# Kernel optimization log

Measured on AMD Instinct MI355X. Metric: run time of the kernel, lower is better.

Reference implementation:

```python
import jax, jax.numpy as jnp
import numpy as np

DIM = 640
HEADS = 8
HEAD_DIM = 80
CROSS = 768
FF_INNER = 4 * DIM  # 2560
EPS = 1e-5
SCALE = HEAD_DIM ** -0.5


def _ln(x, w, b):
    m = jnp.mean(x, axis=-1, keepdims=True)
    v = jnp.var(x, axis=-1, keepdims=True)
    return (x - m) * jax.lax.rsqrt(v + EPS) * w + b


def _split_heads(x):  # [B,S,D] -> [B,H,S,dh]
    B, S, D = x.shape
    return x.reshape(B, S, HEADS, D // HEADS).transpose(0, 2, 1, 3)


def _merge_heads(x):  # [B,H,S,dh] -> [B,S,D]
    B, H, S, dh = x.shape
    return x.transpose(0, 2, 1, 3).reshape(B, S, H * dh)


def _mha(q, k, v):
    # q:[B,S,D] k,v:[B,Skv,D]
    qh, kh, vh = _split_heads(q), _split_heads(k), _split_heads(v)
    scores = jnp.einsum('bhqd,bhkd->bhqk', qh, kh) * SCALE
    probs = jax.nn.softmax(scores, axis=-1)
    out = jnp.einsum('bhqk,bhkd->bhqd', probs, vh)
    return _merge_heads(out)


def _forward(hidden_states, encoder_hidden_states, video_length, p):
    BF, S, D = hidden_states.shape
    f = video_length
    b = BF // f

    # ---- attn1: sparse causal self-attention ----
    x = _ln(hidden_states, p['ln1_w'], p['ln1_b'])
    q = x @ p['q1']
    k = x @ p['k1']
    v = x @ p['v1']
    former = jnp.concatenate([jnp.zeros((1,), jnp.int32), jnp.arange(f - 1, dtype=jnp.int32)])
    def gather_kv(t):  # [BF,S,D] -> [BF,2S,D]
        t = t.reshape(b, f, S, D)
        first = jnp.broadcast_to(t[:, 0:1], (b, f, S, D))
        prev = t[:, former]
        return jnp.concatenate([first, prev], axis=2).reshape(BF, 2 * S, D)
    k = gather_kv(k)
    v = gather_kv(v)
    attn1 = _mha(q, k, v) @ p['o1_w'] + p['o1_b']
    hidden_states = attn1 + hidden_states

    # ---- attn2: cross attention to text ----
    x = _ln(hidden_states, p['ln2_w'], p['ln2_b'])
    q = x @ p['q2']
    k = encoder_hidden_states @ p['k2']
    v = encoder_hidden_states @ p['v2']
    attn2 = _mha(q, k, v) @ p['o2_w'] + p['o2_b']
    hidden_states = attn2 + hidden_states

    # ---- feed-forward (geglu) ----
    x = _ln(hidden_states, p['ln3_w'], p['ln3_b'])
    proj = x @ p['ff_w1'] + p['ff_b1']
    h, gate = jnp.split(proj, 2, axis=-1)
    ff = (h * jax.nn.gelu(gate)) @ p['ff_w2'] + p['ff_b2']
    return ff + hidden_states


def setup_inputs() -> dict:
    key = jax.random.key(0)
    ks = jax.random.split(key, 20)
    s = lambda i, shape, scale=0.02: jax.random.normal(ks[i], shape, jnp.float32) * scale
    inp = {
        'hidden_states': jax.random.normal(ks[0], (8, 1024, DIM), jnp.float32),
        'encoder_hidden_states': jax.random.normal(ks[1], (8, 77, CROSS), jnp.float32),
        'video_length': 8,
        'ln1_w': jnp.ones((DIM,)), 'ln1_b': jnp.zeros((DIM,)),
        'q1': s(2, (DIM, DIM)), 'k1': s(3, (DIM, DIM)), 'v1': s(4, (DIM, DIM)),
        'o1_w': s(5, (DIM, DIM)), 'o1_b': jnp.zeros((DIM,)),
        'ln2_w': jnp.ones((DIM,)), 'ln2_b': jnp.zeros((DIM,)),
        'q2': s(6, (DIM, DIM)), 'k2': s(7, (CROSS, DIM)), 'v2': s(8, (CROSS, DIM)),
        'o2_w': s(9, (DIM, DIM)), 'o2_b': jnp.zeros((DIM,)),
        'ln3_w': jnp.ones((DIM,)), 'ln3_b': jnp.zeros((DIM,)),
        'ff_w1': s(10, (DIM, 2 * FF_INNER)), 'ff_b1': jnp.zeros((2 * FF_INNER,)),
        'ff_w2': s(11, (FF_INNER, DIM)), 'ff_b2': jnp.zeros((DIM,)),
    }
    return inp


def reference(hidden_states, encoder_hidden_states, video_length,
              ln1_w, ln1_b, q1, k1, v1, o1_w, o1_b,
              ln2_w, ln2_b, q2, k2, v2, o2_w, o2_b,
              ln3_w, ln3_b, ff_w1, ff_b1, ff_w2, ff_b2):
    p = dict(ln1_w=ln1_w, ln1_b=ln1_b, q1=q1, k1=k1, v1=v1, o1_w=o1_w, o1_b=o1_b,
             ln2_w=ln2_w, ln2_b=ln2_b, q2=q2, k2=k2, v2=v2, o2_w=o2_w, o2_b=o2_b,
             ln3_w=ln3_w, ln3_b=ln3_b, ff_w1=ff_w1, ff_b1=ff_b1, ff_w2=ff_w2, ff_b2=ff_b2)
    return _forward(hidden_states, encoder_hidden_states, video_length, p)
```

## Files before the change

kernel.cpp:

```cpp
#include <hip/hip_runtime.h>
#include <stdint.h>

#define TOK   8192
#define DIM   640
#define HEADS 8
#define HD    80
#define SEQ   1024
#define CROSS 768
#define ETOK  616
#define FFI   2560
#define SCALE 0.11180339887498949f

typedef unsigned short u16;
typedef unsigned int   u32;

using bf8   = __attribute__((ext_vector_type(8))) short;
using f32x4 = __attribute__((ext_vector_type(4))) float;

struct __align__(16) U4 { u32 x, y, z, w; };
struct __align__(8)  U2 { u32 x, y; };

__device__ __forceinline__ float bf2f(u16 u){
  union { u32 i; float f; } v; v.i = ((u32)u) << 16; return v.f;
}
__device__ __forceinline__ u16 f2bf(float f){
  union { float f; u32 i; } v; v.f = f;
  u32 r = v.i + 0x7fffu + ((v.i >> 16) & 1u);
  return (u16)(r >> 16);
}
__device__ __forceinline__ u32 cvtpk_bf16(float lo, float hi){
  u32 r; asm("v_cvt_pk_bf16_f32 %0, %1, %2" : "=v"(r) : "v"(lo), "v"(hi)); return r;
}
__device__ __forceinline__ float gelu_t(float x){
  float y = 0.7978845608028654f * (x + 0.044715f * x * x * x);
  float e = __expf(2.f * y);
  return 0.5f * x * (2.f - 2.f / (e + 1.f));
}

__device__ __forceinline__ void gl2lds16(const u16* g, u16* l){
  __builtin_amdgcn_global_load_lds(
      (const __attribute__((address_space(1))) void*)g,
      (__attribute__((address_space(3))) void*)l, 16, 0, 0);
}

__global__ void zero_k(u16* p){ p[threadIdx.x] = 0; }

struct CvtJob  { const float* s; u16* d; int n; };
struct CvtJobs { CvtJob j[11]; };
__global__ __launch_bounds__(256) void cvt_all(CvtJobs jobs)
{
  const CvtJob jb = jobs.j[blockIdx.y];
  for (long i = (long)blockIdx.x*256 + threadIdx.x; i < jb.n; i += (long)gridDim.x*256)
    jb.d[i] = f2bf(jb.s[i]);
}

struct TJob  { const float* s; u16* d; int R, C, srcLd, dstLd; };
struct TJobs { TJob j[10]; };
__global__ __launch_bounds__(256) void transpose_tiled(TJobs jobs)
{
  const TJob jb = jobs.j[blockIdx.y];
  const int tilesC = jb.C >> 6;
  const int nt = (jb.R >> 6) * tilesC;
  if ((int)blockIdx.x >= nt) return;
  const int tr = (blockIdx.x / tilesC) << 6, tc = (blockIdx.x % tilesC) << 6;
  __shared__ u16 t[64][65];
  const int tid = threadIdx.x;
  const int rr = tid >> 3, c8 = (tid & 7) * 8;
  #pragma unroll
  for (int p = 0; p < 2; ++p){
    const int r = rr + p*32;
    const float* s = &jb.s[(long)(tr + r)*jb.srcLd + tc + c8];
    #pragma unroll
    for (int j = 0; j < 8; ++j) t[r][c8 + j] = f2bf(s[j]);
  }
  __syncthreads();
  #pragma unroll
  for (int p = 0; p < 2; ++p){
    const int c = rr + p*32;
    u16 tmp[8];
    #pragma unroll
    for (int j = 0; j < 8; ++j) tmp[j] = t[c8 + j][c];
    *(U4*)&jb.d[(long)(tc + c)*jb.dstLd + tr + c8] = *(U4*)tmp;
  }
}

__global__ __launch_bounds__(256) void transpose_tile(
    const u16* __restrict__ src, u16* __restrict__ dst,
    int srcLd, int dstLd)
{
  __shared__ u16 t[64][65];
  const int tr = blockIdx.y << 6, tc = blockIdx.x << 6;
  const int tid = threadIdx.x;
  const int rr = tid >> 3, c8 = (tid & 7) * 8;
  #pragma unroll
  for (int p = 0; p < 2; ++p){
    const int r = rr + p*32;
    U4 v = *(const U4*)&src[(long)(tr + r)*srcLd + tc + c8];
    const u16* pv = (const u16*)&v;
    #pragma unroll
    for (int j = 0; j < 8; ++j) t[r][c8 + j] = pv[j];
  }
  __syncthreads();
  #pragma unroll
  for (int p = 0; p < 2; ++p){
    const int c = rr + p*32;
    u16 tmp[8];
    #pragma unroll
    for (int j = 0; j < 8; ++j) tmp[j] = t[c8 + j][c];
    *(U4*)&dst[(long)(tc + c)*dstLd + tr + c8] = *(U4*)tmp;
  }
}

__global__ __launch_bounds__(256) void transpose_v2(
    const u16* __restrict__ src, u16* __restrict__ dst)
{
  int idx = blockIdx.x*256 + threadIdx.x;
  if (idx >= DIM*640) return;
  int d = idx / 640, c = idx - d*640;
  int g = c / 80, j = c - g*80;
  u16 v = 0;
  if (j < 77) v = src[(long)(g*77 + j)*(2*DIM) + DIM + d];
  dst[(long)d*640 + c] = v;
}

__global__ __launch_bounds__(256) void ln_k(
    const void* __restrict__ src, const u16* __restrict__ w,
    const u16* __restrict__ b, u16* __restrict__ dst, int srcf32)
{
  __shared__ float xr[DIM];
  __shared__ float red[256];
  const int tid = threadIdx.x;
  const long row = blockIdx.x;
  float ls = 0.f;
  for (int i = tid; i < DIM; i += 256){
    float v = srcf32 ? ((const float*)src)[row*DIM + i]
                     : bf2f(((const u16*)src)[row*DIM + i]);
    xr[i] = v; ls += v;
  }
  red[tid] = ls; __syncthreads();
  for (int o = 128; o > 0; o >>= 1){ if (tid < o) red[tid] += red[tid+o]; __syncthreads(); }
  const float mean = red[0] * (1.f/DIM);
  __syncthreads();
  float lq = 0.f;
  for (int i = tid; i < DIM; i += 256){ float d = xr[i] - mean; lq += d*d; }
  red[tid] = lq; __syncthreads();
  for (int o = 128; o > 0; o >>= 1){ if (tid < o) red[tid] += red[tid+o]; __syncthreads(); }
  const float var = red[0] * (1.f/DIM);
  const float rs = rsqrtf(var + 1e-5f);
  u16* q = dst + row*DIM;
  for (int i = tid; i < DIM; i += 256)
    q[i] = f2bf((xr[i] - mean)*rs*bf2f(w[i]) + bf2f(b[i]));
}

template<int BN>
__global__ __launch_bounds__(256) void gemm_bt(
    const u16* __restrict__ A, const u16* __restrict__ BT, void* __restrict__ C,
    int M, int N, int K, int lda, int ldb, int ldc,
    const u16* __restrict__ bias, const void* __restrict__ res, int ldr,
    int resf32, int outf32)
{
  constexpr int NT  = BN/32;
  constexpr int BCH = BN/16;
  constexpr int BPW = BCH/4;
  __shared__ __align__(16) u16 sA[2][8*512];
  __shared__ __align__(16) u16 sB[2][BCH*512];
  const int tid  = threadIdx.x;
  const int wave = tid >> 6, lane = tid & 63;
  const int quad = lane >> 4, l16 = lane & 15;
  const int m0 = blockIdx.y * 128, n0 = blockIdx.x * BN;
  const int wm = (wave >> 1) * 64, wn = (wave & 1) * (BN/2);
  const int srow = lane & 15;
  const int scol = (lane >> 4) * 8;

  long aoff[2];
  #pragma unroll
  for (int i = 0; i < 2; ++i){
    int r = m0 + (wave*2 + i)*16 + srow;
    r = r < M ? r : M - 1;
    aoff[i] = (long)r*lda + scol;
  }
  long boff[BPW];
  #pragma unroll
  for (int i = 0; i < BPW; ++i){
    int r = n0 + (wave*BPW + i)*16 + srow;
    boff[i] = (long)r*ldb + scol;
  }

  f32x4 acc[4][NT] = {};
  #pragma unroll
  for (int i = 0; i < 2; ++i)   gl2lds16(&A[aoff[i]],  &sA[0][(wave*2 + i)*512]);
  #pragma unroll
  for (int i = 0; i < BPW; ++i) gl2lds16(&BT[boff[i]], &sB[0][(wave*BPW + i)*512]);
  __syncthreads();

  int cur = 0;
  for (int k0 = 0; ; ){
    const int kn = k0 + 32;
    if (kn < K){
      #pragma unroll
      for (int i = 0; i < 2; ++i)   gl2lds16(&A[aoff[i] + kn],  &sA[cur^1][(wave*2 + i)*512]);
      #pragma unroll
      for (int i = 0; i < BPW; ++i) gl2lds16(&BT[boff[i] + kn], &sB[cur^1][(wave*BPW + i)*512]);
    }
    bf8 a[4], b[NT];
    #pragma unroll
    for (int mt = 0; mt < 4; ++mt)  a[mt] = *(const bf8*)&sA[cur][((wm>>4) + mt)*512 + lane*8];
    #pragma unroll
    for (int nt = 0; nt < NT; ++nt) b[nt] = *(const bf8*)&sB[cur][((wn>>4) + nt)*512 + lane*8];
    #pragma unroll
    for (int mt = 0; mt < 4; ++mt)
      #pragma unroll
      for (int nt = 0; nt < NT; ++nt)
        acc[mt][nt] = __builtin_amdgcn_mfma_f32_16x16x32_bf16(a[mt], b[nt], acc[mt][nt], 0, 0, 0);
    k0 = kn;
    if (k0 >= K) break;
    __syncthreads();
    cur ^= 1;
  }
  #pragma unroll
  for (int mt = 0; mt < 4; ++mt){
    const int rl = wm + mt*16 + quad*4;
    #pragma unroll
    for (int nt = 0; nt < NT; ++nt){
      const int col = n0 + wn + nt*16 + l16;
      float bv = bias ? bf2f(bias[col]) : 0.f;
      #pragma unroll
      for (int r = 0; r < 4; ++r){
        int row = m0 + rl + r;
        if (row < M){
          float v = acc[mt][nt][r] + bv;
          if (res) v += resf32 ? ((const float*)res)[(long)row*ldr + col]
                               : bf2f(((const u16*)res)[(long)row*ldr + col]);
          if (outf32) ((float*)C)[(long)row*ldc + col] = v;
          else        ((u16*)C) [(long)row*ldc + col] = f2bf(v);
        }
      }
    }
  }
}

__global__ __launch_bounds__(256) void gemm_geglu(
    const u16* __restrict__ A, const u16* __restrict__ W, u16* __restrict__ C,
    const u16* __restrict__ bias)
{
  __shared__ __align__(16) u16 sA[2][8*512];
  __shared__ __align__(16) u16 sH[2][4*512];
  __shared__ __align__(16) u16 sG[2][4*512];
  const int tid  = threadIdx.x;
  const int wave = tid >> 6, lane = tid & 63;
  const int quad = lane >> 4, l16 = lane & 15;
  const int m0 = blockIdx.y * 128, n0 = blockIdx.x * 64;
  const int wm = (wave >> 1) * 64, wn = (wave & 1) * 32;
  const int srow = lane & 15;
  const int scol = (lane >> 4) * 8;

  long aoff[2];
  #pragma unroll
  for (int i = 0; i < 2; ++i)
    aoff[i] = (long)(m0 + (wave*2 + i)*16 + srow)*DIM + scol;
  const long hoff = (long)(n0 + wave*16 + srow)*DIM + scol;
  const long goff = (long)(FFI + n0 + wave*16 + srow)*DIM + scol;

  f32x4 ah[4][2] = {}, ag[4][2] = {};
  #pragma unroll
  for (int i = 0; i < 2; ++i) gl2lds16(&A[aoff[i]], &sA[0][(wave*2 + i)*512]);
  gl2lds16(&W[hoff], &sH[0][wave*512]);
  gl2lds16(&W[goff], &sG[0][wave*512]);
  __syncthreads();

  int cur = 0;
  for (int k0 = 0; ; ){
    const int kn = k0 + 32;
    if (kn < DIM){
      #pragma unroll
      for (int i = 0; i < 2; ++i) gl2lds16(&A[aoff[i] + kn], &sA[cur^1][(wave*2 + i)*512]);
      gl2lds16(&W[hoff + kn], &sH[cur^1][wave*512]);
      gl2lds16(&W[goff + kn], &sG[cur^1][wave*512]);
    }
    bf8 a[4];
    #pragma unroll
    for (int mt = 0; mt < 4; ++mt) a[mt] = *(const bf8*)&sA[cur][((wm>>4) + mt)*512 + lane*8];
    #pragma unroll
    for (int nt = 0; nt < 2; ++nt){
      bf8 bh = *(const bf8*)&sH[cur][((wn>>4) + nt)*512 + lane*8];
      bf8 bg = *(const bf8*)&sG[cur][((wn>>4) + nt)*512 + lane*8];
      #pragma unroll
      for (int mt = 0; mt < 4; ++mt){
        ah[mt][nt] = __builtin_amdgcn_mfma_f32_16x16x32_bf16(a[mt], bh, ah[mt][nt], 0, 0, 0);
        ag[mt][nt] = __builtin_amdgcn_mfma_f32_16x16x32_bf16(a[mt], bg, ag[mt][nt], 0, 0, 0);
      }
    }
    k0 = kn;
    if (k0 >= DIM) break;
    __syncthreads();
    cur ^= 1;
  }
  #pragma unroll
  for (int mt = 0; mt < 4; ++mt){
    const int rl = wm + mt*16 + quad*4;
    #pragma unroll
    for (int nt = 0; nt < 2; ++nt){
      const int col = n0 + wn + nt*16 + l16;
      const float bh = bf2f(bias[col]);
      const float bg = bf2f(bias[FFI + col]);
      #pragma unroll
      for (int r = 0; r < 4; ++r){
        int row = m0 + rl + r;
        float h = ah[mt][nt][r] + bh;
        float g = ag[mt][nt][r] + bg;
        C[(long)row*FFI + col] = f2bf(h * gelu_t(g));
      }
    }
  }
}

template<int MODE>
__global__ __launch_bounds__(256) void attn_k(
    const u16* __restrict__ qbuf, const u16* __restrict__ kbuf,
    const u16* __restrict__ vT, u16* __restrict__ out,
    const u16* __restrict__ zblk)
{
  constexpr int QLD  = MODE ? DIM      : 3*DIM;
  constexpr int KLD  = MODE ? 2*DIM    : 3*DIM;
  constexpr int KCOL = MODE ? 0        : DIM;
  constexpr int VLD  = MODE ? DIM      : TOK;
  constexpr int NK   = MODE ? 77       : 2*SEQ;
  constexpr int NCH  = MODE ? 3        : 64;
  constexpr float C1   = SCALE * 1.4426950408889634f;
  constexpr float THRR = 8.0f / C1;

  const int qt = blockIdx.x, h = blockIdx.y, g = blockIdx.z;
  const int tid = threadIdx.x, wave = tid >> 6, lane = tid & 63;
  const int quad = lane >> 4, l16 = lane & 15;

  __shared__ __align__(16) u16 Qs[64*104];
  __shared__ __align__(16) u16 Kb[6*512];
  __shared__ __align__(16) u16 Vb[5*512];
  __shared__ __align__(16) u16 Ps[4][16*40];

  const int qrow0 = g*SEQ + qt*64;
  for (int v = tid; v < 640; v += 256){
    int r = v/10, c8 = (v - r*10)*8;
    *(U4*)&Qs[r*104 + c8] = *(const U4*)&qbuf[(long)(qrow0 + r)*QLD + h*HD + c8];
  }
  for (int v = tid; v < 128; v += 256){
    U4 z = {0,0,0,0};
    *(U4*)&Qs[(v>>1)*104 + 80 + (v&1)*8] = z;
  }
  __syncthreads();

  bf8 qf[3];
  #pragma unroll
  for (int ks = 0; ks < 3; ++ks)
    qf[ks] = *(const bf8*)&Qs[(wave*16 + l16)*104 + ks*32 + quad*8];

  const int former = (g == 0) ? 0 : (g - 1);

  auto stage = [&](int c){
    int krow0, vrow0;
    if (MODE == 0){
      int kb = c*32;
      int fr = (kb >> 10) ? former : 0;
      krow0 = fr*SEQ + (kb & (SEQ-1));
      vrow0 = krow0;
    } else {
      krow0 = c*32;
      vrow0 = g*80 + c*32;
    }
    #pragma unroll
    for (int ci = 0; ci < 6; ++ci){
      if ((ci & 3) == wave){
        const int ck = ci / 3, ks = ci % 3;
        const int d  = ks*32 + quad*8;
        const int rl = ck*16 + l16;
        const u16* src;
        if (MODE == 0){
          src = (d < HD) ? &kbuf[(long)(krow0 + rl)*KLD + KCOL + h*HD + d] : zblk;
        } else {
          int j = krow0 + rl; j = j < NK ? j : NK-1;
          src = (d < HD) ? &kbuf[((long)g*77 + j)*KLD + KCOL + h*HD + d] : zblk;
        }
        gl2lds16(src, &Kb[ci*512]);
      }
    }
    #pragma unroll
    for (int vi = 0; vi < 5; ++vi){
      if (((vi + 2) & 3) == wave){
        const int dd = vi*16 + l16;
        const u16* src;
        if (MODE == 0){
          src = &vT[(long)(h*HD + dd)*VLD + vrow0 + quad*8];
        } else {
          int key = c*32 + quad*8;
          src = (key < 80) ? &vT[(long)(h*HD + dd)*VLD + vrow0 + quad*8] : zblk;
        }
        gl2lds16(src, &Vb[vi*512]);
      }
    }
  };

  f32x4 o[5] = {};
  float mrun = -1e30f, lrun = 0.f, nmc = 0.f;

  for (int c = 0; c < NCH; ++c){
    stage(c);
    asm volatile("s_waitcnt vmcnt(0)" ::: "memory");
    __syncthreads();

    f32x4 s0 = {}, s1 = {};
    #pragma unroll
    for (int ks = 0; ks < 3; ++ks){
      bf8 kf0 = *(const bf8*)&Kb[ks*512     + lane*8];
      bf8 kf1 = *(const bf8*)&Kb[(3+ks)*512 + lane*8];
      s0 = __builtin_amdgcn_mfma_f32_16x16x32_bf16(kf0, qf[ks], s0, 0, 0, 0);
      s1 = __builtin_amdgcn_mfma_f32_16x16x32_bf16(kf1, qf[ks], s1, 0, 0, 0);
    }

    const int kbase = c*32;
    if (MODE == 1){
      const int kg = kbase + quad*4;
      #pragma unroll
      for (int r = 0; r < 4; ++r){
        if (kg + r >= NK)      s0[r] = -1e30f;
        if (kg + 16 + r >= NK) s1[r] = -1e30f;
      }
    }
    float mxs = fmaxf(fmaxf(fmaxf(s0[0],s0[1]), fmaxf(s0[2],s0[3])),
                      fmaxf(fmaxf(s1[0],s1[1]), fmaxf(s1[2],s1[3])));
    mxs = fmaxf(mxs, __shfl_xor(mxs, 16, 64));
    mxs = fmaxf(mxs, __shfl_xor(mxs, 32, 64));
    if (!__all(mxs - mrun <= THRR)){
      float mn = fmaxf(mrun, mxs);
      float al = exp2f((mrun - mn)*C1);
      mrun = mn; nmc = -mrun*C1;
      lrun *= al;
      float a0 = __shfl(al, quad*4 + 0, 16);
      float a1 = __shfl(al, quad*4 + 1, 16);
      float a2 = __shfl(al, quad*4 + 2, 16);
      float a3 = __shfl(al, quad*4 + 3, 16);
      #pragma unroll
      for (int dt = 0; dt < 5; ++dt){
        o[dt][0] *= a0; o[dt][1] *= a1; o[dt][2] *= a2; o[dt][3] *= a3;
      }
    }
    #pragma unroll
    for (int r = 0; r < 4; ++r){
      s0[r] = exp2f(__builtin_fmaf(s0[r], C1, nmc));
      s1[r] = exp2f(__builtin_fmaf(s1[r], C1, nmc));
    }
    float rs = ((s0[0]+s0[1])+(s0[2]+s0[3])) + ((s1[0]+s1[1])+(s1[2]+s1[3]));
    rs += __shfl_xor(rs, 16, 64);
    rs += __shfl_xor(rs, 32, 64);
    lrun += rs;

    U2 w01, w23;
    w01.x = cvtpk_bf16(s0[0], s0[1]);  w01.y = cvtpk_bf16(s0[2], s0[3]);
    w23.x = cvtpk_bf16(s1[0], s1[1]);  w23.y = cvtpk_bf16(s1[2], s1[3]);
    U2* pr = (U2*)&Ps[wave][l16*40];
    pr[quad]     = w01;
    pr[4 + quad] = w23;
    asm volatile("s_waitcnt lgkmcnt(0)" ::: "memory");
    __builtin_amdgcn_sched_barrier(0);
    bf8 pf = *(const bf8*)&Ps[wave][l16*40 + quad*8];
    #pragma unroll
    for (int dt = 0; dt < 5; ++dt){
      bf8 vf = *(const bf8*)&Vb[dt*512 + lane*8];
      o[dt] = __builtin_amdgcn_mfma_f32_16x16x32_bf16(pf, vf, o[dt], 0, 0, 0);
    }
    __syncthreads();
  }

  float linv[4];
  #pragma unroll
  for (int r = 0; r < 4; ++r)
    linv[r] = __builtin_amdgcn_rcpf(__shfl(lrun, quad*4 + r, 16));
  const int orow0 = qrow0 + wave*16 + quad*4;
  #pragma unroll
  for (int dt = 0; dt < 5; ++dt){
    const int col = h*HD + dt*16 + l16;
    #pragma unroll
    for (int r = 0; r < 4; ++r)
      out[(long)(orow0 + r)*DIM + col] = f2bf(o[dt][r] * linv[r]);
  }
}

extern "C" void kernel_launch(void* const* d_in, const int* in_sizes, int n_in,
                              void* d_out, int out_size, void* d_ws, size_t ws_size,
                              hipStream_t stream)
{
  const float* hidden = (const float*)d_in[0];
  const float* enc    = (const float*)d_in[1];
  const float* ln1w = (const float*)d_in[3],  *ln1b = (const float*)d_in[4];
  const float* q1   = (const float*)d_in[5],  *k1   = (const float*)d_in[6];
  const float* v1   = (const float*)d_in[7],  *o1w  = (const float*)d_in[8];
  const float* o1b  = (const float*)d_in[9];
  const float* ln2w = (const float*)d_in[10], *ln2b = (const float*)d_in[11];
  const float* q2   = (const float*)d_in[12], *k2   = (const float*)d_in[13];
  const float* v2   = (const float*)d_in[14], *o2w  = (const float*)d_in[15];
  const float* o2b  = (const float*)d_in[16];
  const float* ln3w = (const float*)d_in[17], *ln3b = (const float*)d_in[18];
  const float* fw1  = (const float*)d_in[19], *fb1  = (const float*)d_in[20];
  const float* fw2  = (const float*)d_in[21], *fb2  = (const float*)d_in[22];

  u16* ws = (u16*)d_ws;
  u16* Wqkv1T = ws;
  u16* o1T    = Wqkv1T + 1920*640;
  u16* q2T    = o1T    + 640*640;
  u16* Wkv2T  = q2T    + 640*640;
  u16* o2T    = Wkv2T  + 1280*768;
  u16* W1T    = o2T    + 640*640;
  u16* W2T    = W1T    + 5120*640;
  u16* xbuf   = W2T    + 640*2560;
  u16* qkv1   = xbuf   + (size_t)TOK*DIM;
  u16* v1T    = qkv1   + (size_t)TOK*3*DIM;
  u16* ffin   = qkv1;
  u16* attnb  = v1T    + (size_t)DIM*TOK;
  u16* hid2   = attnb  + (size_t)TOK*DIM;
  u16* hid3   = hid2   + (size_t)TOK*DIM;
  u16* q2buf  = hid3   + (size_t)TOK*DIM;
  u16* kv2    = q2buf  + (size_t)TOK*DIM;
  u16* v2T    = kv2    + (size_t)ETOK*2*DIM;
  u16* encm   = v2T    + 640*640 + 64;
  u16* bln1w  = encm   + (size_t)ETOK*CROSS;
  u16* bln1b  = bln1w + DIM;
  u16* bo1b   = bln1b + DIM;
  u16* bln2w  = bo1b  + DIM;
  u16* bln2b  = bln2w + DIM;
  u16* bo2b   = bln2b + DIM;
  u16* bln3w  = bo2b  + DIM;
  u16* bln3b  = bln3w + DIM;
  u16* bfb2   = bln3b + DIM;
  u16* bfb1   = bfb2  + DIM;
  u16* zblk   = bfb1  + 2*FFI;
  u16* wsend  = zblk  + 64;
  const size_t needed = ((size_t)(wsend - ws) + 64) * 2;
  if (ws_size < needed) return;

  dim3 blk(256);
  zero_k<<<1, 64, 0, stream>>>(zblk);

  CvtJobs jobs;
  jobs.j[0]  = { enc,  encm,  ETOK*CROSS };
  jobs.j[1]  = { ln1w, bln1w, DIM };
  jobs.j[2]  = { ln1b, bln1b, DIM };
  jobs.j[3]  = { o1b,  bo1b,  DIM };
  jobs.j[4]  = { ln2w, bln2w, DIM };
  jobs.j[5]  = { ln2b, bln2b, DIM };
  jobs.j[6]  = { o2b,  bo2b,  DIM };
  jobs.j[7]  = { ln3w, bln3w, DIM };
  jobs.j[8]  = { ln3b, bln3b, DIM };
  jobs.j[9]  = { fb2,  bfb2,  DIM };
  jobs.j[10] = { fb1,  bfb1,  2*FFI };
  cvt_all<<<dim3(64,11), blk, 0, stream>>>(jobs);

  TJobs tj;
  tj.j[0] = { q1,  Wqkv1T,            640, 640,  640,  640 };
  tj.j[1] = { k1,  Wqkv1T + 640*640,  640, 640,  640,  640 };
  tj.j[2] = { v1,  Wqkv1T + 1280*640, 640, 640,  640,  640 };
  tj.j[3] = { o1w, o1T,               640, 640,  640,  640 };
  tj.j[4] = { q2,  q2T,               640, 640,  640,  640 };
  tj.j[5] = { k2,  Wkv2T,             768, 640,  640,  768 };
  tj.j[6] = { v2,  Wkv2T + 640*768,   768, 640,  640,  768 };
  tj.j[7] = { o2w, o2T,               640, 640,  640,  640 };
  tj.j[8] = { fw1, W1T,               640, 5120, 5120, 640 };
  tj.j[9] = { fw2, W2T,               2560,640,  640,  2560 };
  transpose_tiled<<<dim3(800,10), blk, 0, stream>>>(tj);

  ln_k<<<TOK, blk, 0, stream>>>(hidden, bln1w, bln1b, xbuf, 1);
  gemm_bt<128><<<dim3(15,64), blk, 0, stream>>>(xbuf, Wqkv1T, qkv1,
      TOK, 3*DIM, DIM, DIM, DIM, 3*DIM, nullptr, nullptr, 0, 0, 0);
  transpose_tile<<<dim3(10,128), blk, 0, stream>>>(qkv1 + 2*DIM, v1T, 3*DIM, TOK);
  attn_k<0><<<dim3(16,8,8), blk, 0, stream>>>(qkv1, qkv1, v1T, attnb, zblk);
  gemm_bt<64><<<dim3(10,64), blk, 0, stream>>>(attnb, o1T, hid2,
      TOK, DIM, DIM, DIM, DIM, DIM, bo1b, hidden, DIM, 1, 0);

  ln_k<<<TOK, blk, 0, stream>>>(hid2, bln2w, bln2b, xbuf, 0);
  gemm_bt<64><<<dim3(10,64), blk, 0, stream>>>(xbuf, q2T, q2buf,
      TOK, DIM, DIM, DIM, DIM, DIM, nullptr, nullptr, 0, 0, 0);
  gemm_bt<64><<<dim3(20,5), blk, 0, stream>>>(encm, Wkv2T, kv2,
      ETOK, 2*DIM, CROSS, CROSS, CROSS, 2*DIM, nullptr, nullptr, 0, 0, 0);
  transpose_v2<<<dim3((DIM*640 + 255)/256), blk, 0, stream>>>(kv2, v2T);
  attn_k<1><<<dim3(16,8,8), blk, 0, stream>>>(q2buf, kv2, v2T, attnb, zblk);
  gemm_bt<64><<<dim3(10,64), blk, 0, stream>>>(attnb, o2T, hid3,
      TOK, DIM, DIM, DIM, DIM, DIM, bo2b, hid2, DIM, 0, 0);

  ln_k<<<TOK, blk, 0, stream>>>(hid3, bln3w, bln3b, xbuf, 0);
  gemm_geglu<<<dim3(40,64), blk, 0, stream>>>(xbuf, W1T, ffin, bfb1);
  gemm_bt<64><<<dim3(10,64), blk, 0, stream>>>(ffin, W2T, d_out,
      TOK, DIM, FFI, FFI, FFI, DIM, bfb2, hid3, DIM, 0, 1);
}
```

Baseline: 726.3 us.

## Enlarge GEMM/GEGLU tiles and process 64-key chunks in attention

The GEGLU GEMM tile grows from 128x64 to 128x128 per block, with 4x4 accumulators per wave for both h and gate. The 640-wide GEMMs switch to the 128-column template variant with half the grid. The attention kernel now handles 64 keys per iteration instead of 32, halving the loop trips and barriers, and precomputes K/V load offsets so the self-attention path avoids per-chunk address math. The trade is more registers and LDS per block, which may cut occupancy, and fewer blocks for the smaller GEMMs (320 blocks).

```diff
diff --git a/kernel.cpp b/kernel.cpp
--- a/kernel.cpp
+++ b/kernel.cpp
@@ -244,28 +244,31 @@
     const u16* __restrict__ bias)
 {
   __shared__ __align__(16) u16 sA[2][8*512];
-  __shared__ __align__(16) u16 sH[2][4*512];
-  __shared__ __align__(16) u16 sG[2][4*512];
+  __shared__ __align__(16) u16 sH[2][8*512];
+  __shared__ __align__(16) u16 sG[2][8*512];
   const int tid  = threadIdx.x;
   const int wave = tid >> 6, lane = tid & 63;
   const int quad = lane >> 4, l16 = lane & 15;
-  const int m0 = blockIdx.y * 128, n0 = blockIdx.x * 64;
-  const int wm = (wave >> 1) * 64, wn = (wave & 1) * 32;
+  const int m0 = blockIdx.y * 128, n0 = blockIdx.x * 128;
+  const int wm = (wave >> 1) * 64, wn = (wave & 1) * 64;
   const int srow = lane & 15;
   const int scol = (lane >> 4) * 8;
 
-  long aoff[2];
-  #pragma unroll
-  for (int i = 0; i < 2; ++i)
+  long aoff[2], hoff[2], goff[2];
+  #pragma unroll
+  for (int i = 0; i < 2; ++i){
     aoff[i] = (long)(m0 + (wave*2 + i)*16 + srow)*DIM + scol;
-  const long hoff = (long)(n0 + wave*16 + srow)*DIM + scol;
-  const long goff = (long)(FFI + n0 + wave*16 + srow)*DIM + scol;
-
-  f32x4 ah[4][2] = {}, ag[4][2] = {};
-  #pragma unroll
-  for (int i = 0; i < 2; ++i) gl2lds16(&A[aoff[i]], &sA[0][(wave*2 + i)*512]);
-  gl2lds16(&W[hoff], &sH[0][wave*512]);
-  gl2lds16(&W[goff], &sG[0][wave*512]);
+    hoff[i] = (long)(n0 + (wave*2 + i)*16 + srow)*DIM + scol;
+    goff[i] = (long)(FFI + n0 + (wave*2 + i)*16 + srow)*DIM + scol;
+  }
+
+  f32x4 ah[4][4] = {}, ag[4][4] = {};
+  #pragma unroll
+  for (int i = 0; i < 2; ++i){
+    gl2lds16(&A[aoff[i]], &sA[0][(wave*2 + i)*512]);
+    gl2lds16(&W[hoff[i]], &sH[0][(wave*2 + i)*512]);
+    gl2lds16(&W[goff[i]], &sG[0][(wave*2 + i)*512]);
+  }
   __syncthreads();
 
   int cur = 0;
@@ -273,15 +276,17 @@
     const int kn = k0 + 32;
     if (kn < DIM){
       #pragma unroll
-      for (int i = 0; i < 2; ++i) gl2lds16(&A[aoff[i] + kn], &sA[cur^1][(wave*2 + i)*512]);
-      gl2lds16(&W[hoff + kn], &sH[cur^1][wave*512]);
-      gl2lds16(&W[goff + kn], &sG[cur^1][wave*512]);
+      for (int i = 0; i < 2; ++i){
+        gl2lds16(&A[aoff[i] + kn], &sA[cur^1][(wave*2 + i)*512]);
+        gl2lds16(&W[hoff[i] + kn], &sH[cur^1][(wave*2 + i)*512]);
+        gl2lds16(&W[goff[i] + kn], &sG[cur^1][(wave*2 + i)*512]);
+      }
     }
     bf8 a[4];
     #pragma unroll
     for (int mt = 0; mt < 4; ++mt) a[mt] = *(const bf8*)&sA[cur][((wm>>4) + mt)*512 + lane*8];
     #pragma unroll
-    for (int nt = 0; nt < 2; ++nt){
+    for (int nt = 0; nt < 4; ++nt){
       bf8 bh = *(const bf8*)&sH[cur][((wn>>4) + nt)*512 + lane*8];
       bf8 bg = *(const bf8*)&sG[cur][((wn>>4) + nt)*512 + lane*8];
       #pragma unroll
@@ -299,7 +304,7 @@
   for (int mt = 0; mt < 4; ++mt){
     const int rl = wm + mt*16 + quad*4;
     #pragma unroll
-    for (int nt = 0; nt < 2; ++nt){
+    for (int nt = 0; nt < 4; ++nt){
       const int col = n0 + wn + nt*16 + l16;
       const float bh = bf2f(bias[col]);
       const float bg = bf2f(bias[FFI + col]);
@@ -325,7 +330,8 @@
   constexpr int KCOL = MODE ? 0        : DIM;
   constexpr int VLD  = MODE ? DIM      : TOK;
   constexpr int NK   = MODE ? 77       : 2*SEQ;
-  constexpr int NCH  = MODE ? 3        : 64;
+  constexpr int NCH  = MODE ? 2        : 32;
+  constexpr int PSTR = 72;
   constexpr float C1   = SCALE * 1.4426950408889634f;
   constexpr float THRR = 8.0f / C1;
 
@@ -334,9 +340,9 @@
   const int quad = lane >> 4, l16 = lane & 15;
 
   __shared__ __align__(16) u16 Qs[64*104];
-  __shared__ __align__(16) u16 Kb[6*512];
-  __shared__ __align__(16) u16 Vb[5*512];
-  __shared__ __align__(16) u16 Ps[4][16*40];
+  __shared__ __align__(16) u16 Kb[12*512];
+  __shared__ __align__(16) u16 Vb[10*512];
+  __shared__ __align__(16) u16 Ps[4][16*PSTR];
 
   const int qrow0 = g*SEQ + qt*64;
   for (int v = tid; v < 640; v += 256){
@@ -356,77 +362,90 @@
 
   const int former = (g == 0) ? 0 : (g - 1);
 
-  auto stage = [&](int c){
-    int krow0, vrow0;
-    if (MODE == 0){
-      int kb = c*32;
-      int fr = (kb >> 10) ? former : 0;
-      krow0 = fr*SEQ + (kb & (SEQ-1));
-      vrow0 = krow0;
-    } else {
-      krow0 = c*32;
-      vrow0 = g*80 + c*32;
-    }
-    #pragma unroll
-    for (int ci = 0; ci < 6; ++ci){
-      if ((ci & 3) == wave){
-        const int ck = ci / 3, ks = ci % 3;
-        const int d  = ks*32 + quad*8;
-        const int rl = ck*16 + l16;
-        const u16* src;
-        if (MODE == 0){
-          src = (d < HD) ? &kbuf[(long)(krow0 + rl)*KLD + KCOL + h*HD + d] : zblk;
-        } else {
-          int j = krow0 + rl; j = j < NK ? j : NK-1;
-          src = (d < HD) ? &kbuf[((long)g*77 + j)*KLD + KCOL + h*HD + d] : zblk;
-        }
-        gl2lds16(src, &Kb[ci*512]);
-      }
-    }
-    #pragma unroll
-    for (int vi = 0; vi < 5; ++vi){
-      if (((vi + 2) & 3) == wave){
-        const int dd = vi*16 + l16;
-        const u16* src;
-        if (MODE == 0){
-          src = &vT[(long)(h*HD + dd)*VLD + vrow0 + quad*8];
-        } else {
-          int key = c*32 + quad*8;
-          src = (key < 80) ? &vT[(long)(h*HD + dd)*VLD + vrow0 + quad*8] : zblk;
-        }
-        gl2lds16(src, &Vb[vi*512]);
-      }
-    }
-  };
+  long ko[3], koB[3], vo[3], voB[3];
+  bool koob[3];
+  if (MODE == 0){
+    #pragma unroll
+    for (int j = 0; j < 3; ++j){
+      const int ci = wave + 4*j;
+      const int kgj = ci/3, ksj = ci - kgj*3;
+      const int d = ksj*32 + quad*8;
+      koob[j] = (d >= HD);
+      const int dcl = koob[j] ? 0 : d;
+      const int row = kgj*16 + l16;
+      ko[j]  = (long)row*KLD + KCOL + h*HD + dcl;
+      koB[j] = (long)(former*SEQ + row)*KLD + KCOL + h*HD + dcl;
+      const int dtj = ci >> 1, khj = ci & 1;
+      vo[j]  = (long)(h*HD + dtj*16 + l16)*VLD + khj*32 + quad*8;
+      voB[j] = vo[j] + (long)former*SEQ;
+    }
+  }
 
   f32x4 o[5] = {};
   float mrun = -1e30f, lrun = 0.f, nmc = 0.f;
 
   for (int c = 0; c < NCH; ++c){
-    stage(c);
+    if (MODE == 0){
+      if (c == 16){
+        #pragma unroll
+        for (int j = 0; j < 3; ++j){ ko[j] = koB[j]; vo[j] = voB[j]; }
+      }
+      #pragma unroll
+      for (int j = 0; j < 3; ++j)
+        gl2lds16(koob[j] ? zblk : &kbuf[ko[j]], &Kb[(wave + 4*j)*512]);
+      #pragma unroll
+      for (int j = 0; j < 3; ++j)
+        if (wave + 4*j < 10) gl2lds16(&vT[vo[j]], &Vb[(wave + 4*j)*512]);
+      #pragma unroll
+      for (int j = 0; j < 3; ++j){ ko[j] += 64L*KLD; vo[j] += 64; }
+    } else {
+      #pragma unroll
+      for (int j = 0; j < 3; ++j){
+        const int ci = wave + 4*j;
+        const int kgj = ci/3, ksj = ci - kgj*3;
+        const int d = ksj*32 + quad*8;
+        int row = c*64 + kgj*16 + l16; row = row < NK ? row : NK-1;
+        const u16* src = (d < HD) ? &kbuf[((long)g*77 + row)*KLD + KCOL + h*HD + d] : zblk;
+        gl2lds16(src, &Kb[ci*512]);
+      }
+      #pragma unroll
+      for (int j = 0; j < 3; ++j){
+        const int vi = wave + 4*j;
+        if (vi < 10){
+          const int dtj = vi >> 1, khj = vi & 1;
+          const int key = c*64 + khj*32 + quad*8;
+          const u16* src = (key < 80)
+              ? &vT[(long)(h*HD + dtj*16 + l16)*VLD + g*80 + key] : zblk;
+          gl2lds16(src, &Vb[vi*512]);
+        }
+      }
+    }
     asm volatile("s_waitcnt vmcnt(0)" ::: "memory");
     __syncthreads();
 
-    f32x4 s0 = {}, s1 = {};
-    #pragma unroll
-    for (int ks = 0; ks < 3; ++ks){
-      bf8 kf0 = *(const bf8*)&Kb[ks*512     + lane*8];
-      bf8 kf1 = *(const bf8*)&Kb[(3+ks)*512 + lane*8];
-      s0 = __builtin_amdgcn_mfma_f32_16x16x32_bf16(kf0, qf[ks], s0, 0, 0, 0);
-      s1 = __builtin_amdgcn_mfma_f32_16x16x32_bf16(kf1, qf[ks], s1, 0, 0, 0);
-    }
-
-    const int kbase = c*32;
+    f32x4 s[4] = {};
+    #pragma unroll
+    for (int kgi = 0; kgi < 4; ++kgi)
+      #pragma unroll
+      for (int ksi = 0; ksi < 3; ++ksi){
+        bf8 kf = *(const bf8*)&Kb[(kgi*3 + ksi)*512 + lane*8];
+        s[kgi] = __builtin_amdgcn_mfma_f32_16x16x32_bf16(kf, qf[ksi], s[kgi], 0, 0, 0);
+      }
+
+    const int kbase = c*64;
     if (MODE == 1){
-      const int kg = kbase + quad*4;
-      #pragma unroll
-      for (int r = 0; r < 4; ++r){
-        if (kg + r >= NK)      s0[r] = -1e30f;
-        if (kg + 16 + r >= NK) s1[r] = -1e30f;
-      }
-    }
-    float mxs = fmaxf(fmaxf(fmaxf(s0[0],s0[1]), fmaxf(s0[2],s0[3])),
-                      fmaxf(fmaxf(s1[0],s1[1]), fmaxf(s1[2],s1[3])));
+      #pragma unroll
+      for (int kgi = 0; kgi < 4; ++kgi){
+        const int kg0 = kbase + kgi*16 + quad*4;
+        #pragma unroll
+        for (int r = 0; r < 4; ++r)
+          if (kg0 + r >= NK) s[kgi][r] = -1e30f;
+      }
+    }
+    float mxs = -1e30f;
+    #pragma unroll
+    for (int kgi = 0; kgi < 4; ++kgi)
+      mxs = fmaxf(mxs, fmaxf(fmaxf(s[kgi][0], s[kgi][1]), fmaxf(s[kgi][2], s[kgi][3])));
     mxs = fmaxf(mxs, __shfl_xor(mxs, 16, 64));
     mxs = fmaxf(mxs, __shfl_xor(mxs, 32, 64));
     if (!__all(mxs - mrun <= THRR)){
@@ -443,29 +462,35 @@
         o[dt][0] *= a0; o[dt][1] *= a1; o[dt][2] *= a2; o[dt][3] *= a3;
       }
     }
-    #pragma unroll
-    for (int r = 0; r < 4; ++r){
-      s0[r] = exp2f(__builtin_fmaf(s0[r], C1, nmc));
-      s1[r] = exp2f(__builtin_fmaf(s1[r], C1, nmc));
-    }
-    float rs = ((s0[0]+s0[1])+(s0[2]+s0[3])) + ((s1[0]+s1[1])+(s1[2]+s1[3]));
+    float rs = 0.f;
+    #pragma unroll
+    for (int kgi = 0; kgi < 4; ++kgi){
+      #pragma unroll
+      for (int r = 0; r < 4; ++r)
+        s[kgi][r] = exp2f(__builtin_fmaf(s[kgi][r], C1, nmc));
+      rs += (s[kgi][0] + s[kgi][1]) + (s[kgi][2] + s[kgi][3]);
+    }
     rs += __shfl_xor(rs, 16, 64);
     rs += __shfl_xor(rs, 32, 64);
     lrun += rs;
 
-    U2 w01, w23;
-    w01.x = cvtpk_bf16(s0[0], s0[1]);  w01.y = cvtpk_bf16(s0[2], s0[3]);
-    w23.x = cvtpk_bf16(s1[0], s1[1]);  w23.y = cvtpk_bf16(s1[2], s1[3]);
-    U2* pr = (U2*)&Ps[wave][l16*40];
-    pr[quad]     = w01;
-    pr[4 + quad] = w23;
+    #pragma unroll
+    for (int kgi = 0; kgi < 4; ++kgi){
+      U2 w;
+      w.x = cvtpk_bf16(s[kgi][0], s[kgi][1]);
+      w.y = cvtpk_bf16(s[kgi][2], s[kgi][3]);
+      *(U2*)&Ps[wave][l16*PSTR + kgi*16 + quad*4] = w;
+    }
     asm volatile("s_waitcnt lgkmcnt(0)" ::: "memory");
     __builtin_amdgcn_sched_barrier(0);
-    bf8 pf = *(const bf8*)&Ps[wave][l16*40 + quad*8];
-    #pragma unroll
-    for (int dt = 0; dt < 5; ++dt){
-      bf8 vf = *(const bf8*)&Vb[dt*512 + lane*8];
-      o[dt] = __builtin_amdgcn_mfma_f32_16x16x32_bf16(pf, vf, o[dt], 0, 0, 0);
+    #pragma unroll
+    for (int kh = 0; kh < 2; ++kh){
+      bf8 pf = *(const bf8*)&Ps[wave][l16*PSTR + kh*32 + quad*8];
+      #pragma unroll
+      for (int dt = 0; dt < 5; ++dt){
+        bf8 vf = *(const bf8*)&Vb[(dt*2 + kh)*512 + lane*8];
+        o[dt] = __builtin_amdgcn_mfma_f32_16x16x32_bf16(pf, vf, o[dt], 0, 0, 0);
+      }
     }
     __syncthreads();
   }
@@ -571,21 +596,21 @@
       TOK, 3*DIM, DIM, DIM, DIM, 3*DIM, nullptr, nullptr, 0, 0, 0);
   transpose_tile<<<dim3(10,128), blk, 0, stream>>>(qkv1 + 2*DIM, v1T, 3*DIM, TOK);
   attn_k<0><<<dim3(16,8,8), blk, 0, stream>>>(qkv1, qkv1, v1T, attnb, zblk);
-  gemm_bt<64><<<dim3(10,64), blk, 0, stream>>>(attnb, o1T, hid2,
+  gemm_bt<128><<<dim3(5,64), blk, 0, stream>>>(attnb, o1T, hid2,
       TOK, DIM, DIM, DIM, DIM, DIM, bo1b, hidden, DIM, 1, 0);
 
   ln_k<<<TOK, blk, 0, stream>>>(hid2, bln2w, bln2b, xbuf, 0);
-  gemm_bt<64><<<dim3(10,64), blk, 0, stream>>>(xbuf, q2T, q2buf,
+  gemm_bt<128><<<dim3(5,64), blk, 0, stream>>>(xbuf, q2T, q2buf,
       TOK, DIM, DIM, DIM, DIM, DIM, nullptr, nullptr, 0, 0, 0);
-  gemm_bt<64><<<dim3(20,5), blk, 0, stream>>>(encm, Wkv2T, kv2,
+  gemm_bt<128><<<dim3(10,5), blk, 0, stream>>>(encm, Wkv2T, kv2,
       ETOK, 2*DIM, CROSS, CROSS, CROSS, 2*DIM, nullptr, nullptr, 0, 0, 0);
   transpose_v2<<<dim3((DIM*640 + 255)/256), blk, 0, stream>>>(kv2, v2T);
   attn_k<1><<<dim3(16,8,8), blk, 0, stream>>>(q2buf, kv2, v2T, attnb, zblk);
-  gemm_bt<64><<<dim3(10,64), blk, 0, stream>>>(attnb, o2T, hid3,
+  gemm_bt<128><<<dim3(5,64), blk, 0, stream>>>(attnb, o2T, hid3,
       TOK, DIM, DIM, DIM, DIM, DIM, bo2b, hid2, DIM, 0, 0);
 
   ln_k<<<TOK, blk, 0, stream>>>(hid3, bln3w, bln3b, xbuf, 0);
-  gemm_geglu<<<dim3(40,64), blk, 0, stream>>>(xbuf, W1T, ffin, bfb1);
-  gemm_bt<64><<<dim3(10,64), blk, 0, stream>>>(ffin, W2T, d_out,
+  gemm_geglu<<<dim3(20,64), blk, 0, stream>>>(xbuf, W1T, ffin, bfb1);
+  gemm_bt<128><<<dim3(5,64), blk, 0, stream>>>(ffin, W2T, d_out,
       TOK, DIM, FFI, FFI, FFI, DIM, bfb2, hid3, DIM, 0, 1);
 }
```

Measured after the change: 868.4 us. 1.2x slower.
